# Kernel tuning notes

Hardware: AMD Instinct MI355X
Metric: run time of the kernel (lower is better)

The kernel has to match this reference:

```python
import jax, jax.numpy as jnp
from jax import lax
import numpy as np


def conv2d(x, w, pad):
    # x: NCHW, w: OIHW
    return lax.conv_general_dilated(
        x, w, window_strides=(1, 1), padding=[(pad, pad), (pad, pad)],
        dimension_numbers=("NCHW", "OIHW", "NCHW"))


def _scan_dir(x, a, axis, reverse):
    """Directional IRNN scan: cur = relu(x_i + alpha * prev), prev0 = 0.
    a broadcasts as (1, C, 1) over the remaining (B, C, L) slice dims."""
    if reverse:
        x = jnp.flip(x, axis)
    xs = jnp.moveaxis(x, axis, 0)  # (L, B, C, other)

    def step(prev, xi):
        cur = jax.nn.relu(xi + a * prev)
        return cur, cur

    _, hs = lax.scan(step, jnp.zeros_like(xs[0]), xs)
    h = jnp.moveaxis(hs, 0, axis)
    if reverse:
        h = jnp.flip(h, axis)
    return h


def spatial_irnn(x, alpha):
    a = alpha.reshape(1, -1, 1)  # broadcasts over (B, C, W) or (B, C, H)
    h_td = _scan_dir(x, a, axis=2, reverse=False)  # top -> down
    h_dt = _scan_dir(x, a, axis=2, reverse=True)   # down -> top
    h_lr = _scan_dir(x, a, axis=3, reverse=False)  # left -> right
    h_rl = _scan_dir(x, a, axis=3, reverse=True)   # right -> left
    return h_td, h_lr, h_dt, h_rl


def setup_inputs() -> dict:
    key = jax.random.key(0)
    ks = jax.random.split(key, 10)
    B, C, H, W = 8, 32, 256, 256
    mid = C // 2
    s = 0.05
    return {
        "x": jax.random.normal(ks[0], (B, C, H, W), jnp.float32),
        "alpha1": jnp.full((C,), 0.2, jnp.float32),
        "alpha2": jnp.full((C,), 0.2, jnp.float32),
        "w_in": jax.random.normal(ks[1], (C, C, 3, 3), jnp.float32) * s,
        "w2": jax.random.normal(ks[2], (C, 4 * C, 3, 3), jnp.float32) * s,
        "w3": jax.random.normal(ks[3], (C, 4 * C, 3, 3), jnp.float32) * s,
        "att_w1": jax.random.normal(ks[4], (mid, C, 3, 3), jnp.float32) * s,
        "att_w2": jax.random.normal(ks[5], (mid, mid, 3, 3), jnp.float32) * s,
        "att_w3": jax.random.normal(ks[6], (4, mid, 1, 1), jnp.float32) * s,
        "att_b3": jnp.zeros((4,), jnp.float32),
        "w_out": jax.random.normal(ks[7], (1, C, 1, 1), jnp.float32) * s,
    }


def reference(x, alpha1, alpha2, w_in, w2, w3, att_w1, att_w2, att_w3, att_b3, w_out):
    # Attention gate: 4 per-direction weight maps in (0,1)
    a = jax.nn.relu(conv2d(x, att_w1, pad=1))
    a = jax.nn.relu(conv2d(a, att_w2, pad=1))
    weight = jax.nn.sigmoid(conv2d(a, att_w3, pad=0) + att_b3.reshape(1, -1, 1, 1))

    def gate(up, right, down, left):
        return jnp.concatenate([
            up * weight[:, 0:1], right * weight[:, 1:2],
            down * weight[:, 2:3], left * weight[:, 3:4]], axis=1)

    out = conv2d(x, w_in, pad=1)
    up, right, down, left = spatial_irnn(out, alpha1)
    out = conv2d(gate(up, right, down, left), w2, pad=1)
    up, right, down, left = spatial_irnn(out, alpha2)
    out = jax.nn.relu(conv2d(gate(up, right, down, left), w3, pad=1))
    mask = jax.nn.sigmoid(conv2d(out, w_out, pad=0))
    return mask
```

## Files before the change

### kernel.cpp

```cpp
#include <hip/hip_runtime.h>
#include <cstddef>

#define H_ 256
#define W_ 256
#define HW_ 65536

typedef unsigned int uint;
typedef unsigned short ushort;
typedef __attribute__((ext_vector_type(8))) short short8;
typedef __attribute__((ext_vector_type(16))) float floatx16;

__device__ __forceinline__ float bf2f(ushort u) {
    return __uint_as_float(((uint)u) << 16);
}
__device__ __forceinline__ ushort f2bf(float f) {
    uint u = __float_as_uint(f);
    uint r = (u + 0x7fffu + ((u >> 16) & 1u)) >> 16;
    return (ushort)r;
}
__device__ __forceinline__ float sigmoidf_(float x) {
    return 1.0f / (1.0f + expf(-x));
}

__device__ __forceinline__ void prep_one(const float* src, ushort* dst,
                                         int CO, int CI, int e) {
    int chunk = e / 9216;
    int r = e - chunk * 9216;
    int co = r / 288;
    int kk = r - co * 288;
    int khw = kk >> 5;
    int ci = kk & 31;
    int cig = chunk * 32 + ci;
    float v = 0.f;
    if (co < CO && cig < CI) v = src[(co * CI + cig) * 9 + khw];
    int s = kk >> 4;
    int lane = ((kk >> 3) & 1) * 32 + co;
    int j = kk & 7;
    dst[(((size_t)chunk * 18 + s) * 64 + lane) * 8 + j] = f2bf(v);
}

__global__ __launch_bounds__(256) void prep_weights(
    const float* __restrict__ w_in, const float* __restrict__ w2,
    const float* __restrict__ w3, const float* __restrict__ aw1,
    const float* __restrict__ aw2,
    ushort* __restrict__ w_inB, ushort* __restrict__ w2B,
    ushort* __restrict__ w3B, ushort* __restrict__ aw1B,
    ushort* __restrict__ aw2B, ushort* __restrict__ zp) {
    int idx = blockIdx.x * 256 + threadIdx.x;
    if (idx < 64) zp[idx] = 0;
    if (idx < 9216)        prep_one(w_in, w_inB, 32, 32, idx);
    else if (idx < 46080)  prep_one(w2, w2B, 32, 128, idx - 9216);
    else if (idx < 82944)  prep_one(w3, w3B, 32, 128, idx - 46080);
    else if (idx < 92160)  prep_one(aw1, aw1B, 16, 32, idx - 82944);
    else if (idx < 101376) prep_one(aw2, aw2B, 16, 16, idx - 92160);
}

__global__ __launch_bounds__(256) void transform_x(const float* __restrict__ x,
                                                   ushort* __restrict__ xh) {
    __shared__ float s[64][33];
    const int t = threadIdx.x;
    const int w0 = blockIdx.x * 64, h = blockIdx.y, b = blockIdx.z;
    {
        int ww = t & 63, c0 = (t >> 6) * 8;
#pragma unroll
        for (int j = 0; j < 8; j++) {
            int c = c0 + j;
            s[ww][c] = x[((size_t)(b * 32 + c)) * HW_ + h * W_ + w0 + ww];
        }
    }
    __syncthreads();
    {
        int p = t >> 2, cb = t & 3;
        ushort tmp[8];
#pragma unroll
        for (int j = 0; j < 8; j++) tmp[j] = f2bf(s[p][cb * 8 + j]);
        *(uint4*)(xh + (((size_t)b * HW_ + h * W_ + w0 + p) * 32) + cb * 8) =
            *(const uint4*)tmp;
    }
}

struct StageDesc {
    uint goff[6];
    int slot[6];
    bool ok[6];
};
__device__ __forceinline__ void make_desc(StageDesc& d, int t, int w0, int h0, int b) {
#pragma unroll
    for (int i = 0; i < 6; i++) {
        int u = i * 256 + t;
        int row = u / 136;
        int rem = u - row * 136;
        int p = rem >> 2, cb = rem & 3;
        int gh = h0 - 1 + row, gw = w0 - 1 + p;
        d.ok[i] = (u < 1360) && ((unsigned)gh < 256u) && ((unsigned)gw < 256u);
        d.goff[i] = d.ok[i] ? (((uint)b * HW_ + (uint)gh * W_ + (uint)gw) * 32 + cb * 8) : 0u;
        d.slot[i] = row * 136 + (p << 2) + (cb ^ (p & 3) ^ ((p >> 2) & 3));
    }
}
__device__ __forceinline__ void stage6(ushort* smem, const StageDesc& d,
                                       const ushort* __restrict__ inp,
                                       const ushort* __restrict__ zp, int t) {
    uint4 v[6];
#pragma unroll
    for (int i = 0; i < 6; i++) {
        const ushort* src = d.ok[i] ? (inp + d.goff[i]) : zp;
        v[i] = *(const uint4*)src;
    }
#pragma unroll
    for (int i = 0; i < 6; i++) {
        if (i * 256 + t < 1360) *(uint4*)(smem + (size_t)d.slot[i] * 8) = v[i];
    }
}
__device__ __forceinline__ void mfma_chunk(const ushort* smem, const ushort* wbp,
                                           int lco, int lhalf, int wid,
                                           floatx16& acc0, floatx16& acc1) {
#pragma unroll
    for (int half = 0; half < 2; half++) {
        short8 bf[9];
#pragma unroll
        for (int j = 0; j < 9; j++)
            bf[j] = *(const short8*)(wbp + (size_t)(2 * j + half) * 512);
        const int cbr = half * 2 + lhalf;
#pragma unroll
        for (int kw = 0; kw < 3; kw++) {
            const int ww = lco + kw;
            const int cbs = cbr ^ (ww & 3) ^ ((ww >> 2) & 3);
            short8 a[4];
#pragma unroll
            for (int r = 0; r < 4; r++)
                a[r] = *(const short8*)(smem + (size_t)((wid * 2 + r) * 136 + (ww << 2) + cbs) * 8);
#pragma unroll
            for (int kh = 0; kh < 3; kh++) {
                acc0 = __builtin_amdgcn_mfma_f32_32x32x16_bf16(a[kh], bf[kh * 3 + kw], acc0, 0, 0, 0);
                acc1 = __builtin_amdgcn_mfma_f32_32x32x16_bf16(a[kh + 1], bf[kh * 3 + kw], acc1, 0, 0, 0);
            }
        }
    }
}

template<int NCHUNK, int EPI, bool RELU>
__global__ __launch_bounds__(256, 4) void conv_mfma(
    const ushort* __restrict__ in0, const ushort* __restrict__ in1,
    const ushort* __restrict__ in2, const ushort* __restrict__ in3,
    const ushort* __restrict__ wB, const ushort* __restrict__ zp,
    ushort* __restrict__ outp, const float* __restrict__ aux_w,
    const float* __restrict__ aux_b) {
    __shared__ __align__(16) ushort smem[1360 * 8];
    const int t = threadIdx.x;
    const int wid = t >> 6;
    const int lane = t & 63;
    const int lco = lane & 31, lhalf = lane >> 5;
    const int w0 = blockIdx.x * 32, h0 = blockIdx.y * 8, b = blockIdx.z;
    const ushort* ins[4] = {in0, in1, in2, in3};

    StageDesc d;
    make_desc(d, t, w0, h0, b);

    floatx16 acc0, acc1;
#pragma unroll
    for (int i = 0; i < 16; i++) { acc0[i] = 0.f; acc1[i] = 0.f; }

#pragma unroll
    for (int ch = 0; ch < NCHUNK; ch++) {
        __syncthreads();
        stage6(smem, d, ins[ch], zp, t);
        __syncthreads();
        mfma_chunk(smem, wB + ((size_t)ch * 18 * 64 + lane) * 8, lco, lhalf, wid,
                   acc0, acc1);
    }

    if (EPI == 0) {
#pragma unroll
        for (int r = 0; r < 16; r++) {
            int wl = (r & 3) + 8 * (r >> 2) + 4 * lhalf;
            float v0 = acc0[r], v1 = acc1[r];
            if (RELU) { v0 = fmaxf(v0, 0.f); v1 = fmaxf(v1, 0.f); }
            size_t p0 = (((size_t)b * HW_ + (h0 + wid * 2) * W_ + w0 + wl) * 32) + lco;
            outp[p0] = f2bf(v0);
            outp[p0 + (size_t)W_ * 32] = f2bf(v1);
        }
    } else {
        __syncthreads();
#pragma unroll
        for (int r = 0; r < 16; r++) {
            int wl = (r & 3) + 8 * (r >> 2) + 4 * lhalf;
            float v0 = acc0[r], v1 = acc1[r];
            if (RELU) { v0 = fmaxf(v0, 0.f); v1 = fmaxf(v1, 0.f); }
            int pix0 = (wid * 2) * 32 + wl;
            smem[(size_t)pix0 * 40 + lco] = f2bf(v0);
            smem[(size_t)(pix0 + 32) * 40 + lco] = f2bf(v1);
        }
        __syncthreads();
        const ushort* tp = smem + (size_t)t * 40;
        if (EPI == 1) {
            float xin[16];
            uint4 q0 = *(const uint4*)tp;
            uint4 q1 = *(const uint4*)(tp + 8);
            const ushort* u0 = (const ushort*)&q0;
            const ushort* u1 = (const ushort*)&q1;
#pragma unroll
            for (int j = 0; j < 8; j++) { xin[j] = bf2f(u0[j]); xin[8 + j] = bf2f(u1[j]); }
            size_t pix = (size_t)b * HW_ + (size_t)(h0 + (t >> 5)) * W_ + w0 + (t & 31);
#pragma unroll
            for (int g = 0; g < 4; g++) {
                float acc = aux_b[g];
#pragma unroll
                for (int ci = 0; ci < 16; ci++) acc = fmaf(xin[ci], aux_w[g * 16 + ci], acc);
                outp[(size_t)g * 8 * HW_ + pix] = f2bf(sigmoidf_(acc));
            }
        } else {
            float acc = 0.f;
#pragma unroll
            for (int q = 0; q < 4; q++) {
                uint4 qv = *(const uint4*)(tp + q * 8);
                const ushort* uq = (const ushort*)&qv;
#pragma unroll
                for (int j = 0; j < 8; j++) acc = fmaf(bf2f(uq[j]), aux_w[q * 8 + j], acc);
            }
            float* fo = (float*)outp;
            fo[(size_t)b * HW_ + (size_t)(h0 + (t >> 5)) * W_ + w0 + (t & 31)] = sigmoidf_(acc);
        }
    }
}

__global__ __launch_bounds__(256, 4) void conv_dual(
    const ushort* __restrict__ in0, const ushort* __restrict__ wBa,
    const ushort* __restrict__ wBb, const ushort* __restrict__ zp,
    ushort* __restrict__ outA, ushort* __restrict__ outB) {
    __shared__ __align__(16) ushort smem[1360 * 8];
    const int t = threadIdx.x;
    const int wid = t >> 6;
    const int lane = t & 63;
    const int lco = lane & 31, lhalf = lane >> 5;
    const int w0 = blockIdx.x * 32, h0 = blockIdx.y * 8, b = blockIdx.z;

    StageDesc d;
    make_desc(d, t, w0, h0, b);

    floatx16 accA0, accA1, accB0, accB1;
#pragma unroll
    for (int i = 0; i < 16; i++) { accA0[i] = 0.f; accA1[i] = 0.f; accB0[i] = 0.f; accB1[i] = 0.f; }

    stage6(smem, d, in0, zp, t);
    __syncthreads();
    mfma_chunk(smem, wBa + (size_t)lane * 8, lco, lhalf, wid, accA0, accA1);
    mfma_chunk(smem, wBb + (size_t)lane * 8, lco, lhalf, wid, accB0, accB1);

#pragma unroll
    for (int r = 0; r < 16; r++) {
        int wl = (r & 3) + 8 * (r >> 2) + 4 * lhalf;
        size_t p0 = (((size_t)b * HW_ + (h0 + wid * 2) * W_ + w0 + wl) * 32) + lco;
        outA[p0] = f2bf(accA0[r]);
        outA[p0 + (size_t)W_ * 32] = f2bf(accA1[r]);
        outB[p0] = f2bf(fmaxf(accB0[r], 0.f));
        outB[p0 + (size_t)W_ * 32] = f2bf(fmaxf(accB1[r], 0.f));
    }
}

template<int VERT>
__device__ __forceinline__ void scan_body(
    const ushort* __restrict__ feat, const float* __restrict__ alpha,
    const ushort* __restrict__ wmapT, ushort* __restrict__ gfwd,
    ushort* __restrict__ gbwd, int gf, int gb, int bx, int t) {
    const int cg = t & 3;
    const int col = (bx & 3) * 64 + (t >> 2);
    const int seg = (bx >> 2) & 7;
    const int dir = (bx >> 5) & 1;
    const int b = bx >> 6;
    const int c0 = cg * 8;

    float a[8];
#pragma unroll
    for (int j = 0; j < 8; j++) a[j] = alpha[c0 + j];

    const ushort* wplane = wmapT + (size_t)(dir ? gb : gf) * 8 * HW_ + (size_t)b * HW_;
    ushort* gout = dir ? gbwd : gfwd;

    const int main0 = seg * 32;
    const int start = (seg == 0) ? 0 : main0 - 16;
    const int cnt = main0 - start + 32;

    auto pixof = [&](int p) -> size_t {
        int phys = dir ? 255 - p : p;
        return VERT ? ((size_t)phys * W_ + col) : ((size_t)col * W_ + phys);
    };

    uint4 xv[4];
    ushort wv[4];
#pragma unroll
    for (int k = 0; k < 4; k++) {
        size_t pix = pixof(start + k);
        xv[k] = *(const uint4*)(feat + ((size_t)b * HW_ + pix) * 32 + c0);
        wv[k] = wplane[pix];
    }
    float prev[8];
#pragma unroll
    for (int j = 0; j < 8; j++) prev[j] = 0.f;

    for (int i = 0; i < cnt; i += 4) {
#pragma unroll
        for (int k = 0; k < 4; k++) {
            const int p = start + i + k;
            uint4 xcur = xv[k];
            ushort wcur = wv[k];
            if (i + k + 4 < cnt) {
                size_t pix = pixof(p + 4);
                xv[k] = *(const uint4*)(feat + ((size_t)b * HW_ + pix) * 32 + c0);
                wv[k] = wplane[pix];
            }
            const ushort* xu = (const ushort*)&xcur;
            if (p >= main0) {
                float wmv = bf2f(wcur);
                ushort o[8];
#pragma unroll
                for (int j = 0; j < 8; j++) {
                    float cur = fmaxf(fmaf(a[j], prev[j], bf2f(xu[j])), 0.f);
                    prev[j] = cur;
                    o[j] = f2bf(cur * wmv);
                }
                *(uint4*)(gout + ((size_t)b * HW_ + pixof(p)) * 32 + c0) = *(const uint4*)o;
            } else {
#pragma unroll
                for (int j = 0; j < 8; j++)
                    prev[j] = fmaxf(fmaf(a[j], prev[j], bf2f(xu[j])), 0.f);
            }
        }
    }
}

__global__ __launch_bounds__(256) void scan_both(
    const ushort* __restrict__ feat, const float* __restrict__ alpha,
    const ushort* __restrict__ wmapT, ushort* __restrict__ g0,
    ushort* __restrict__ g1, ushort* __restrict__ g2, ushort* __restrict__ g3) {
    const int bx = blockIdx.x & 511;
    if (blockIdx.x < 512)
        scan_body<1>(feat, alpha, wmapT, g0, g2, 0, 2, bx, threadIdx.x);
    else
        scan_body<0>(feat, alpha, wmapT, g1, g3, 1, 3, bx, threadIdx.x);
}

extern "C" void kernel_launch(void* const* d_in, const int* in_sizes, int n_in,
                              void* d_out, int out_size, void* d_ws, size_t ws_size,
                              hipStream_t stream) {
    const float* x      = (const float*)d_in[0];
    const float* alpha1 = (const float*)d_in[1];
    const float* alpha2 = (const float*)d_in[2];
    const float* w_in   = (const float*)d_in[3];
    const float* w2     = (const float*)d_in[4];
    const float* w3     = (const float*)d_in[5];
    const float* aw1    = (const float*)d_in[6];
    const float* aw2    = (const float*)d_in[7];
    const float* aw3    = (const float*)d_in[8];
    const float* ab3    = (const float*)d_in[9];
    const float* wout   = (const float*)d_in[10];
    float* out = (float*)d_out;

    const size_t TEN = (size_t)8 * HW_ * 32;
    ushort* p = (ushort*)d_ws;
    ushort* xh    = p; p += TEN;
    ushort* feat  = p; p += TEN;
    ushort* g0    = p; p += TEN;
    ushort* g1    = p; p += TEN;
    ushort* g2    = p; p += TEN;
    ushort* g3    = p; p += TEN;
    ushort* wmapT = p; p += (size_t)4 * 8 * HW_;
    ushort* w_inB = p; p += 9216;
    ushort* w2B   = p; p += 36864;
    ushort* w3B   = p; p += 36864;
    ushort* aw1B  = p; p += 9216;
    ushort* aw2B  = p; p += 9216;
    ushort* zp    = p; p += 64;
    ushort* a1z   = g1;

    prep_weights<<<396, 256, 0, stream>>>(w_in, w2, w3, aw1, aw2,
                                          w_inB, w2B, w3B, aw1B, aw2B, zp);
    transform_x<<<dim3(4, 256, 8), 256, 0, stream>>>(x, xh);

    dim3 gconv(8, 32, 8);

    conv_dual<<<gconv, 256, 0, stream>>>(xh, w_inB, aw1B, zp, feat, a1z);
    conv_mfma<1, 1, true><<<gconv, 256, 0, stream>>>(a1z, a1z, a1z, a1z, aw2B, zp,
                                                     wmapT, aw3, ab3);

    scan_both<<<1024, 256, 0, stream>>>(feat, alpha1, wmapT, g0, g1, g2, g3);

    conv_mfma<4, 0, false><<<gconv, 256, 0, stream>>>(g0, g1, g2, g3, w2B, zp,
                                                      feat, nullptr, nullptr);

    scan_both<<<1024, 256, 0, stream>>>(feat, alpha2, wmapT, g0, g1, g2, g3);

    conv_mfma<4, 2, true><<<gconv, 256, 0, stream>>>(g0, g1, g2, g3, w3B, zp,
                                                     (ushort*)out, wout, nullptr);
}
```

Before: 377.8 us.

## Stage conv tiles with direct global-to-LDS loads and double buffering

Replaces register-staged tile loads with `global_load_lds` 16-byte transfers that write straight into shared memory. The XOR swizzle moves from the LDS slot to the global source offset. The multi-chunk conv kernel now double-buffers its shared tiles, so the load of the next input chunk is issued before computing the current one, and one barrier per chunk is dropped. This is meant to hide global load latency and save VGPRs. In exchange, LDS use per block roughly doubles for multi-chunk kernels, which may lower occupancy.

```diff
diff --git a/kernel.cpp b/kernel.cpp
--- a/kernel.cpp
+++ b/kernel.cpp
@@ -21,6 +21,11 @@
 __device__ __forceinline__ float sigmoidf_(float x) {
     return 1.0f / (1.0f + expf(-x));
 }
+
+#define GLOAD_LDS16(gsrc, ldst)                                                   \
+    __builtin_amdgcn_global_load_lds(                                             \
+        (const __attribute__((address_space(1))) void*)(gsrc),                    \
+        (__attribute__((address_space(3))) void*)(ldst), 16, 0, 0)
 
 __device__ __forceinline__ void prep_one(const float* src, ushort* dst,
                                          int CO, int CI, int e) {
@@ -79,38 +84,33 @@
     }
 }
 
-struct StageDesc {
+struct StageDescL {
     uint goff[6];
-    int slot[6];
     bool ok[6];
 };
-__device__ __forceinline__ void make_desc(StageDesc& d, int t, int w0, int h0, int b) {
+__device__ __forceinline__ void make_descL(StageDescL& d, int t, int w0, int h0, int b) {
 #pragma unroll
     for (int i = 0; i < 6; i++) {
         int u = i * 256 + t;
         int row = u / 136;
         int rem = u - row * 136;
-        int p = rem >> 2, cb = rem & 3;
+        int p = rem >> 2, q = rem & 3;
+        int cb = q ^ (p & 3) ^ ((p >> 2) & 3);
         int gh = h0 - 1 + row, gw = w0 - 1 + p;
         d.ok[i] = (u < 1360) && ((unsigned)gh < 256u) && ((unsigned)gw < 256u);
         d.goff[i] = d.ok[i] ? (((uint)b * HW_ + (uint)gh * W_ + (uint)gw) * 32 + cb * 8) : 0u;
-        d.slot[i] = row * 136 + (p << 2) + (cb ^ (p & 3) ^ ((p >> 2) & 3));
-    }
-}
-__device__ __forceinline__ void stage6(ushort* smem, const StageDesc& d,
-                                       const ushort* __restrict__ inp,
-                                       const ushort* __restrict__ zp, int t) {
-    uint4 v[6];
+    }
+}
+__device__ __forceinline__ void stage_lds(ushort* smem, const StageDescL& d,
+                                          const ushort* __restrict__ inp,
+                                          const ushort* __restrict__ zp, int t) {
 #pragma unroll
     for (int i = 0; i < 6; i++) {
         const ushort* src = d.ok[i] ? (inp + d.goff[i]) : zp;
-        v[i] = *(const uint4*)src;
-    }
-#pragma unroll
-    for (int i = 0; i < 6; i++) {
-        if (i * 256 + t < 1360) *(uint4*)(smem + (size_t)d.slot[i] * 8) = v[i];
-    }
-}
+        GLOAD_LDS16(src, smem + (size_t)(i * 256 + t) * 8);
+    }
+}
+
 __device__ __forceinline__ void mfma_chunk(const ushort* smem, const ushort* wbp,
                                            int lco, int lhalf, int wid,
                                            floatx16& acc0, floatx16& acc1) {
@@ -145,7 +145,8 @@
     const ushort* __restrict__ wB, const ushort* __restrict__ zp,
     ushort* __restrict__ outp, const float* __restrict__ aux_w,
     const float* __restrict__ aux_b) {
-    __shared__ __align__(16) ushort smem[1360 * 8];
+    constexpr int NBUF = (NCHUNK > 1) ? 2 : 1;
+    __shared__ __align__(16) ushort smem[NBUF][1536 * 8];
     const int t = threadIdx.x;
     const int wid = t >> 6;
     const int lane = t & 63;
@@ -153,20 +154,22 @@
     const int w0 = blockIdx.x * 32, h0 = blockIdx.y * 8, b = blockIdx.z;
     const ushort* ins[4] = {in0, in1, in2, in3};
 
-    StageDesc d;
-    make_desc(d, t, w0, h0, b);
+    StageDescL d;
+    make_descL(d, t, w0, h0, b);
 
     floatx16 acc0, acc1;
 #pragma unroll
     for (int i = 0; i < 16; i++) { acc0[i] = 0.f; acc1[i] = 0.f; }
+
+    stage_lds(smem[0], d, ins[0], zp, t);
 
 #pragma unroll
     for (int ch = 0; ch < NCHUNK; ch++) {
         __syncthreads();
-        stage6(smem, d, ins[ch], zp, t);
-        __syncthreads();
-        mfma_chunk(smem, wB + ((size_t)ch * 18 * 64 + lane) * 8, lco, lhalf, wid,
-                   acc0, acc1);
+        if (ch + 1 < NCHUNK)
+            stage_lds(smem[(ch + 1) & 1], d, ins[ch + 1], zp, t);
+        mfma_chunk(smem[ch & 1], wB + ((size_t)ch * 18 * 64 + lane) * 8,
+                   lco, lhalf, wid, acc0, acc1);
     }
 
     if (EPI == 0) {
@@ -181,17 +184,18 @@
         }
     } else {
         __syncthreads();
+        ushort* ep = &smem[0][0];
 #pragma unroll
         for (int r = 0; r < 16; r++) {
             int wl = (r & 3) + 8 * (r >> 2) + 4 * lhalf;
             float v0 = acc0[r], v1 = acc1[r];
             if (RELU) { v0 = fmaxf(v0, 0.f); v1 = fmaxf(v1, 0.f); }
             int pix0 = (wid * 2) * 32 + wl;
-            smem[(size_t)pix0 * 40 + lco] = f2bf(v0);
-            smem[(size_t)(pix0 + 32) * 40 + lco] = f2bf(v1);
+            ep[(size_t)pix0 * 40 + lco] = f2bf(v0);
+            ep[(size_t)(pix0 + 32) * 40 + lco] = f2bf(v1);
         }
         __syncthreads();
-        const ushort* tp = smem + (size_t)t * 40;
+        const ushort* tp = ep + (size_t)t * 40;
         if (EPI == 1) {
             float xin[16];
             uint4 q0 = *(const uint4*)tp;
@@ -227,21 +231,21 @@
     const ushort* __restrict__ in0, const ushort* __restrict__ wBa,
     const ushort* __restrict__ wBb, const ushort* __restrict__ zp,
     ushort* __restrict__ outA, ushort* __restrict__ outB) {
-    __shared__ __align__(16) ushort smem[1360 * 8];
+    __shared__ __align__(16) ushort smem[1536 * 8];
     const int t = threadIdx.x;
     const int wid = t >> 6;
     const int lane = t & 63;
     const int lco = lane & 31, lhalf = lane >> 5;
     const int w0 = blockIdx.x * 32, h0 = blockIdx.y * 8, b = blockIdx.z;
 
-    StageDesc d;
-    make_desc(d, t, w0, h0, b);
+    StageDescL d;
+    make_descL(d, t, w0, h0, b);
 
     floatx16 accA0, accA1, accB0, accB1;
 #pragma unroll
     for (int i = 0; i < 16; i++) { accA0[i] = 0.f; accA1[i] = 0.f; accB0[i] = 0.f; accB1[i] = 0.f; }
 
-    stage6(smem, d, in0, zp, t);
+    stage_lds(smem, d, in0, zp, t);
     __syncthreads();
     mfma_chunk(smem, wBa + (size_t)lane * 8, lco, lhalf, wid, accA0, accA1);
     mfma_chunk(smem, wBb + (size_t)lane * 8, lco, lhalf, wid, accB0, accB1);
```

Result: slower. 386.9 us (+2.4%).
